# Performance work log

Measured on AMD Instinct MI355X. Metric: run time of the kernel, lower is better.

## Reference

```python
import jax, jax.numpy as jnp
import numpy as np

EPS = 1e-9

def setup_inputs() -> dict:
    key = jax.random.key(0)
    k1, k2 = jax.random.split(key)
    B, D = 65536, 512
    e = jax.random.normal(k1, (B, D), dtype=jnp.float32)
    tau = jax.random.normal(k2, (B, D), dtype=jnp.float32)
    return {"e": e, "tau": tau}

def reference(e, tau):
    # Barlow Twins (diagonal-only) loss.
    # torch .std(dim=0) is unbiased (ddof=1).
    B = e.shape[0]
    e_norm = (e - e.mean(axis=0)) / (e.std(axis=0, ddof=1) + EPS)
    tau_norm = (tau - tau.mean(axis=0)) / (tau.std(axis=0, ddof=1) + EPS)
    # diag(e_norm.T @ tau_norm) / B == per-feature batch reduction of products
    c_diag = jnp.sum(e_norm * tau_norm, axis=0) / B
    return jnp.sum((1.0 - c_diag) ** 2)
```

## Files before the change

### kernel.cpp

```cpp
#include <hip/hip_runtime.h>

#define BT_D  512
#define BT_D4 128
#define NBLK  1024
#define NTHR  256
#define BT_U  8

#define BT_ACC(ev, tv)                                                  \
    do {                                                                \
        se.x += (ev).x; se.y += (ev).y; se.z += (ev).z; se.w += (ev).w; \
        st.x += (tv).x; st.y += (tv).y; st.z += (tv).z; st.w += (tv).w; \
        se2.x = fmaf((ev).x, (ev).x, se2.x);                            \
        se2.y = fmaf((ev).y, (ev).y, se2.y);                            \
        se2.z = fmaf((ev).z, (ev).z, se2.z);                            \
        se2.w = fmaf((ev).w, (ev).w, se2.w);                            \
        st2.x = fmaf((tv).x, (tv).x, st2.x);                            \
        st2.y = fmaf((tv).y, (tv).y, st2.y);                            \
        st2.z = fmaf((tv).z, (tv).z, st2.z);                            \
        st2.w = fmaf((tv).w, (tv).w, st2.w);                            \
        set.x = fmaf((ev).x, (tv).x, set.x);                            \
        set.y = fmaf((ev).y, (tv).y, set.y);                            \
        set.z = fmaf((ev).z, (tv).z, set.z);                            \
        set.w = fmaf((ev).w, (tv).w, set.w);                            \
    } while (0)

__global__ __launch_bounds__(NTHR, 4) void bt_partial_kernel(
    const float4* __restrict__ e4, const float4* __restrict__ t4,
    float* __restrict__ acc, int B, int nslot)
{
    const int tid = threadIdx.x;
    const int c4  = tid & (BT_D4 - 1);
    const int r   = tid >> 7;

    float4 se  = make_float4(0.f, 0.f, 0.f, 0.f);
    float4 se2 = make_float4(0.f, 0.f, 0.f, 0.f);
    float4 st  = make_float4(0.f, 0.f, 0.f, 0.f);
    float4 st2 = make_float4(0.f, 0.f, 0.f, 0.f);
    float4 set = make_float4(0.f, 0.f, 0.f, 0.f);

    const size_t T  = (size_t)gridDim.x * NTHR;
    const size_t N4 = (size_t)B * BT_D4;
    size_t i = (size_t)blockIdx.x * NTHR + tid;

    for (; i + (BT_U - 1) * T < N4; i += BT_U * T) {
        float4 ev[BT_U], tv[BT_U];
#pragma unroll
        for (int u = 0; u < BT_U; ++u) {
            ev[u] = e4[i + u * T];
            tv[u] = t4[i + u * T];
        }
#pragma unroll
        for (int u = 0; u < BT_U; ++u) BT_ACC(ev[u], tv[u]);
    }
    for (; i < N4; i += T) {
        const float4 ev = e4[i];
        const float4 tv = t4[i];
        BT_ACC(ev, tv);
    }

    __shared__ float4 lds[BT_D4][5];
    if (r == 1) {
        lds[c4][0] = se;  lds[c4][1] = se2; lds[c4][2] = st;
        lds[c4][3] = st2; lds[c4][4] = set;
    }
    __syncthreads();
    if (r == 0) {
        float4 a;
        a = lds[c4][0]; se.x += a.x; se.y += a.y; se.z += a.z; se.w += a.w;
        a = lds[c4][1]; se2.x += a.x; se2.y += a.y; se2.z += a.z; se2.w += a.w;
        a = lds[c4][2]; st.x += a.x; st.y += a.y; st.z += a.z; st.w += a.w;
        a = lds[c4][3]; st2.x += a.x; st2.y += a.y; st2.z += a.z; st2.w += a.w;
        a = lds[c4][4]; set.x += a.x; set.y += a.y; set.z += a.z; set.w += a.w;

        float* ap = acc + (size_t)(blockIdx.x % nslot) * (5 * BT_D);
        const int col = c4 * 4;
        atomicAdd(&ap[0 * BT_D + col + 0], se.x);
        atomicAdd(&ap[0 * BT_D + col + 1], se.y);
        atomicAdd(&ap[0 * BT_D + col + 2], se.z);
        atomicAdd(&ap[0 * BT_D + col + 3], se.w);
        atomicAdd(&ap[1 * BT_D + col + 0], se2.x);
        atomicAdd(&ap[1 * BT_D + col + 1], se2.y);
        atomicAdd(&ap[1 * BT_D + col + 2], se2.z);
        atomicAdd(&ap[1 * BT_D + col + 3], se2.w);
        atomicAdd(&ap[2 * BT_D + col + 0], st.x);
        atomicAdd(&ap[2 * BT_D + col + 1], st.y);
        atomicAdd(&ap[2 * BT_D + col + 2], st.z);
        atomicAdd(&ap[2 * BT_D + col + 3], st.w);
        atomicAdd(&ap[3 * BT_D + col + 0], st2.x);
        atomicAdd(&ap[3 * BT_D + col + 1], st2.y);
        atomicAdd(&ap[3 * BT_D + col + 2], st2.z);
        atomicAdd(&ap[3 * BT_D + col + 3], st2.w);
        atomicAdd(&ap[4 * BT_D + col + 0], set.x);
        atomicAdd(&ap[4 * BT_D + col + 1], set.y);
        atomicAdd(&ap[4 * BT_D + col + 2], set.z);
        atomicAdd(&ap[4 * BT_D + col + 3], set.w);
    }
}

__global__ __launch_bounds__(512) void bt_final_kernel(
    const float* __restrict__ acc, float* __restrict__ out, int B, int nslot)
{
    const int d = threadIdx.x;
    double Se = 0, Se2 = 0, St = 0, St2 = 0, Set = 0;
    for (int s = 0; s < nslot; ++s) {
        const float* a = acc + (size_t)s * (5 * BT_D);
        Se  += a[0 * BT_D + d];
        Se2 += a[1 * BT_D + d];
        St  += a[2 * BT_D + d];
        St2 += a[3 * BT_D + d];
        Set += a[4 * BT_D + d];
    }
    const double Bd = (double)B;
    const double me = Se / Bd, mt = St / Bd;
    double ve = (Se2 - Bd * me * me) / (Bd - 1.0);
    double vt = (St2 - Bd * mt * mt) / (Bd - 1.0);
    ve = ve > 0.0 ? ve : 0.0;
    vt = vt > 0.0 ? vt : 0.0;
    const double sd_e = sqrt(ve) + 1e-9;
    const double sd_t = sqrt(vt) + 1e-9;
    const double c = (Set - Bd * me * mt) / (sd_e * sd_t * Bd);
    const double v = (1.0 - c) * (1.0 - c);

    __shared__ double red[BT_D];
    red[d] = v;
    __syncthreads();
    for (int s = BT_D / 2; s > 0; s >>= 1) {
        if (d < s) red[d] += red[d + s];
        __syncthreads();
    }
    if (d == 0) out[0] = (float)red[0];
}

extern "C" void kernel_launch(void* const* d_in, const int* in_sizes, int n_in,
                              void* d_out, int out_size, void* d_ws, size_t ws_size,
                              hipStream_t stream) {
    const float* e   = (const float*)d_in[0];
    const float* tau = (const float*)d_in[1];
    const int B = in_sizes[0] / BT_D;
    float* acc = (float*)d_ws;

    int nslot = 1;
    const size_t slot_bytes = (size_t)5 * BT_D * sizeof(float);
    if (ws_size >= 32 * slot_bytes)      nslot = 32;
    else if (ws_size >= 8 * slot_bytes)  nslot = 8;
    else if (ws_size >= 4 * slot_bytes)  nslot = 4;
    else if (ws_size >= 2 * slot_bytes)  nslot = 2;

    (void)hipMemsetAsync(d_ws, 0, (size_t)nslot * slot_bytes, stream);

    bt_partial_kernel<<<NBLK, NTHR, 0, stream>>>(
        (const float4*)e, (const float4*)tau, acc, B, nslot);
    bt_final_kernel<<<1, BT_D, 0, stream>>>(acc, (float*)d_out, B, nslot);
}
```

Before: 291.5 us.

## Double block size, shrink unroll, use 32-bit indexing, and parallelize final reduction

The partial kernel now uses 512 threads per block with unroll 2 instead of 8, 32-bit indices, and a two-stage LDS tree reduction. The aim is lower register pressure and higher occupancy while still streaming both inputs. The final kernel is split across 8 wavefront-sized blocks using shuffle reductions and a float atomicAdd into an output that is zeroed beforehand, which removes the single-block LDS tree. This adds an extra memset launch, and the output sum now depends on atomic ordering.

New measurement: 287.5 us. Within noise of the previous version (-1.3%).

```diff
diff --git a/kernel.cpp b/kernel.cpp
--- a/kernel.cpp
+++ b/kernel.cpp
@@ -3,8 +3,8 @@
 #define BT_D  512
 #define BT_D4 128
 #define NBLK  1024
-#define NTHR  256
-#define BT_U  8
+#define NTHR  512
+#define BT_U  2
 
 #define BT_ACC(ev, tv)                                                  \
     do {                                                                \
@@ -24,7 +24,10 @@
         set.w = fmaf((ev).w, (tv).w, set.w);                            \
     } while (0)
 
-__global__ __launch_bounds__(NTHR, 4) void bt_partial_kernel(
+#define BT_ADD4(dst, a) \
+    do { (dst).x += (a).x; (dst).y += (a).y; (dst).z += (a).z; (dst).w += (a).w; } while (0)
+
+__global__ __launch_bounds__(NTHR, 8) void bt_partial_kernel(
     const float4* __restrict__ e4, const float4* __restrict__ t4,
     float* __restrict__ acc, int B, int nslot)
 {
@@ -38,19 +41,17 @@
     float4 st2 = make_float4(0.f, 0.f, 0.f, 0.f);
     float4 set = make_float4(0.f, 0.f, 0.f, 0.f);
 
-    const size_t T  = (size_t)gridDim.x * NTHR;
-    const size_t N4 = (size_t)B * BT_D4;
-    size_t i = (size_t)blockIdx.x * NTHR + tid;
+    const unsigned T  = (unsigned)gridDim.x * NTHR;
+    const unsigned N4 = (unsigned)B * BT_D4;
+    unsigned i = (unsigned)blockIdx.x * NTHR + tid;
 
-    for (; i + (BT_U - 1) * T < N4; i += BT_U * T) {
-        float4 ev[BT_U], tv[BT_U];
-#pragma unroll
-        for (int u = 0; u < BT_U; ++u) {
-            ev[u] = e4[i + u * T];
-            tv[u] = t4[i + u * T];
-        }
-#pragma unroll
-        for (int u = 0; u < BT_U; ++u) BT_ACC(ev[u], tv[u]);
+    for (; i + T < N4; i += BT_U * T) {
+        const float4 e0 = e4[i];
+        const float4 t0 = t4[i];
+        const float4 e1 = e4[i + T];
+        const float4 t1 = t4[i + T];
+        BT_ACC(e0, t0);
+        BT_ACC(e1, t1);
     }
     for (; i < N4; i += T) {
         const float4 ev = e4[i];
@@ -58,21 +59,30 @@
         BT_ACC(ev, tv);
     }
 
-    __shared__ float4 lds[BT_D4][5];
+    __shared__ float4 lds[2][BT_D4][5];
+    if (r >= 2) {
+        float4 (*L)[5] = lds[r - 2];
+        L[c4][0] = se;  L[c4][1] = se2; L[c4][2] = st;
+        L[c4][3] = st2; L[c4][4] = set;
+    }
+    __syncthreads();
+    if (r < 2) {
+        float4 (*L)[5] = lds[r];
+        BT_ADD4(se,  L[c4][0]); BT_ADD4(se2, L[c4][1]); BT_ADD4(st, L[c4][2]);
+        BT_ADD4(st2, L[c4][3]); BT_ADD4(set, L[c4][4]);
+    }
+    __syncthreads();
     if (r == 1) {
-        lds[c4][0] = se;  lds[c4][1] = se2; lds[c4][2] = st;
-        lds[c4][3] = st2; lds[c4][4] = set;
+        lds[0][c4][0] = se;  lds[0][c4][1] = se2; lds[0][c4][2] = st;
+        lds[0][c4][3] = st2; lds[0][c4][4] = set;
     }
     __syncthreads();
     if (r == 0) {
-        float4 a;
-        a = lds[c4][0]; se.x += a.x; se.y += a.y; se.z += a.z; se.w += a.w;
-        a = lds[c4][1]; se2.x += a.x; se2.y += a.y; se2.z += a.z; se2.w += a.w;
-        a = lds[c4][2]; st.x += a.x; st.y += a.y; st.z += a.z; st.w += a.w;
-        a = lds[c4][3]; st2.x += a.x; st2.y += a.y; st2.z += a.z; st2.w += a.w;
-        a = lds[c4][4]; set.x += a.x; set.y += a.y; set.z += a.z; set.w += a.w;
+        BT_ADD4(se,  lds[0][c4][0]); BT_ADD4(se2, lds[0][c4][1]);
+        BT_ADD4(st,  lds[0][c4][2]); BT_ADD4(st2, lds[0][c4][3]);
+        BT_ADD4(set, lds[0][c4][4]);
 
-        float* ap = acc + (size_t)(blockIdx.x % nslot) * (5 * BT_D);
+        float* ap = acc + (size_t)(blockIdx.x & (nslot - 1)) * (5 * BT_D);
         const int col = c4 * 4;
         atomicAdd(&ap[0 * BT_D + col + 0], se.x);
         atomicAdd(&ap[0 * BT_D + col + 1], se.y);
@@ -97,11 +107,12 @@
     }
 }
 
-__global__ __launch_bounds__(512) void bt_final_kernel(
+__global__ __launch_bounds__(64) void bt_final_kernel(
     const float* __restrict__ acc, float* __restrict__ out, int B, int nslot)
 {
-    const int d = threadIdx.x;
+    const int d = blockIdx.x * 64 + threadIdx.x;
     double Se = 0, Se2 = 0, St = 0, St2 = 0, Set = 0;
+#pragma unroll 4
     for (int s = 0; s < nslot; ++s) {
         const float* a = acc + (size_t)s * (5 * BT_D);
         Se  += a[0 * BT_D + d];
@@ -119,16 +130,12 @@
     const double sd_e = sqrt(ve) + 1e-9;
     const double sd_t = sqrt(vt) + 1e-9;
     const double c = (Set - Bd * me * mt) / (sd_e * sd_t * Bd);
-    const double v = (1.0 - c) * (1.0 - c);
+    double v = (1.0 - c) * (1.0 - c);
 
-    __shared__ double red[BT_D];
-    red[d] = v;
-    __syncthreads();
-    for (int s = BT_D / 2; s > 0; s >>= 1) {
-        if (d < s) red[d] += red[d + s];
-        __syncthreads();
-    }
-    if (d == 0) out[0] = (float)red[0];
+    for (int off = 32; off > 0; off >>= 1)
+        v += __shfl_down(v, off, 64);
+    if (threadIdx.x == 0)
+        atomicAdd(out, (float)v);
 }
 
 extern "C" void kernel_launch(void* const* d_in, const int* in_sizes, int n_in,
@@ -147,8 +154,9 @@
     else if (ws_size >= 2 * slot_bytes)  nslot = 2;
 
     (void)hipMemsetAsync(d_ws, 0, (size_t)nslot * slot_bytes, stream);
+    (void)hipMemsetAsync(d_out, 0, sizeof(float), stream);
 
     bt_partial_kernel<<<NBLK, NTHR, 0, stream>>>(
         (const float4*)e, (const float4*)tau, acc, B, nslot);
-    bt_final_kernel<<<1, BT_D, 0, stream>>>(acc, (float*)d_out, B, nslot);
+    bt_final_kernel<<<8, 64, 0, stream>>>(acc, (float*)d_out, B, nslot);
 }
```
